# Optimization experiments

Measured on AMD Instinct MI355X. Metric: run time of the kernel, lower is better.

The kernel has to match this reference:

```python
import jax, jax.numpy as jnp
import numpy as np

N_NODES = 100000
N_EDGES = 3200000
D = 128
B = 4


def gcn_conv(x, row, col, W, b, n):
    # PyG GCNConv: x' = D^{-1/2}(A+I)D^{-1/2} (x W) + b
    xw = x @ W  # [N, out]
    ones = jnp.ones((row.shape[0],), dtype=x.dtype)
    deg = jax.ops.segment_sum(ones, col, num_segments=n) + 1.0  # self-loop
    dinv = jax.lax.rsqrt(deg)  # deg > 0 because of self-loops
    norm = dinv[row] * dinv[col]  # [E]
    msg = xw[row] * norm[:, None]  # gather + scale
    agg = jax.ops.segment_sum(msg, col, num_segments=n)  # scatter-add
    agg = agg + (dinv * dinv)[:, None] * xw  # self-loop contribution
    return agg + b


def setup_inputs() -> dict:
    key = jax.random.key(0)
    ks = jax.random.split(key, 10)
    x = jax.random.normal(ks[0], (N_NODES, D), dtype=jnp.float32)
    edge_index = jax.random.randint(ks[1], (2, N_EDGES), 0, N_NODES, dtype=jnp.int64)
    question_embeddings = jax.random.normal(ks[2], (B, D), dtype=jnp.float32)
    s = 1.0 / np.sqrt(D)
    W1 = jax.random.uniform(ks[3], (D, D), jnp.float32, -s, s)
    b1 = jnp.zeros((D,), jnp.float32)
    W2 = jax.random.uniform(ks[4], (D, D), jnp.float32, -s, s)
    b2 = jnp.zeros((D,), jnp.float32)
    Wq = jax.random.uniform(ks[5], (D, D), jnp.float32, -s, s)
    bq = jax.random.uniform(ks[6], (D,), jnp.float32, -s, s)
    return {"x": x, "edge_index": edge_index, "question_embeddings": question_embeddings,
            "W1": W1, "b1": b1, "W2": W2, "b2": b2, "Wq": Wq, "bq": bq}


def reference(x, edge_index, question_embeddings, W1, b1, W2, b2, Wq, bq):
    n = x.shape[0]
    row, col = edge_index[0], edge_index[1]
    h = jax.nn.relu(gcn_conv(x, row, col, W1, b1, n))  # [N, H]
    h = gcn_conv(h, row, col, W2, b2, n)  # [N, H]
    q = question_embeddings @ Wq + bq  # [B, H]
    out = h[None, :, :] + q[:, None, :]  # [B, N, H]
    return jax.nn.log_softmax(out, axis=1)  # softmax over node dim (torch dim=1)
```

## Files before the change

kernel.cpp:

```cpp
#include <hip/hip_runtime.h>
#include <math.h>

#define DD 128
#define CT 16384
#define CAP 10240

typedef unsigned int uint;
typedef unsigned short u16;

typedef __attribute__((ext_vector_type(8))) __bf16 bf16x8;
typedef __attribute__((ext_vector_type(2))) __bf16 bf16x2;
typedef __attribute__((ext_vector_type(4))) float f32x4;
typedef __attribute__((ext_vector_type(4))) uint uint4v;
typedef __attribute__((ext_vector_type(8))) u16 u16x8;


__device__ inline uint bf16bits(float a) {
  uint u = __float_as_uint(a);
  return (u + 0x7fffu + ((u >> 16) & 1u)) >> 16;
}

__device__ inline uint pack_bf16x2(float a, float b) {
  bf16x2 t;
  t[0] = (__bf16)a;
  t[1] = (__bf16)b;
  return __builtin_bit_cast(uint, t);
}

__device__ inline float lo16f(uint u) { return __uint_as_float(u << 16); }
__device__ inline float hi16f(uint u) { return __uint_as_float(u & 0xffff0000u); }


__global__ __launch_bounds__(256) void k_coarse(const int* __restrict__ row,
                                                const int* __restrict__ col,
                                                int* __restrict__ gcursor,
                                                uint* __restrict__ coarse,
                                                int E, int NB) {
  __shared__ int hist[512];
  __shared__ int base[512];
  int tid = threadIdx.x;
  long e0 = (long)blockIdx.x * CT;
  int cnt = (int)min((long)CT, (long)E - e0);
  int cnt4 = cnt >> 2;
  const int4* c4p = (const int4*)(col + e0);
  const int4* r4p = (const int4*)(row + e0);
  for (int i = tid; i < NB; i += 256) hist[i] = 0;
  __syncthreads();
  for (int i = tid; i < cnt4; i += 256) {
    int4 c = c4p[i];
    atomicAdd(&hist[c.x >> 8], 1);
    atomicAdd(&hist[c.y >> 8], 1);
    atomicAdd(&hist[c.z >> 8], 1);
    atomicAdd(&hist[c.w >> 8], 1);
  }
  for (int i = (cnt4 << 2) + tid; i < cnt; i += 256) atomicAdd(&hist[col[e0 + i] >> 8], 1);
  __syncthreads();
  for (int i = tid; i < NB; i += 256) {
    base[i] = i * CAP + atomicAdd(&gcursor[i], hist[i]);
    hist[i] = 0;
  }
  __syncthreads();
  for (int i = tid; i < cnt4; i += 256) {
    int4 c = c4p[i];
    int4 r = r4p[i];
    int b;
    b = c.x >> 8; coarse[base[b] + atomicAdd(&hist[b], 1)] = ((uint)r.x << 8) | (uint)(c.x & 255);
    b = c.y >> 8; coarse[base[b] + atomicAdd(&hist[b], 1)] = ((uint)r.y << 8) | (uint)(c.y & 255);
    b = c.z >> 8; coarse[base[b] + atomicAdd(&hist[b], 1)] = ((uint)r.z << 8) | (uint)(c.z & 255);
    b = c.w >> 8; coarse[base[b] + atomicAdd(&hist[b], 1)] = ((uint)r.w << 8) | (uint)(c.w & 255);
  }
  for (int i = (cnt4 << 2) + tid; i < cnt; i += 256) {
    int c = col[e0 + i];
    int r = row[e0 + i];
    int b = c >> 8;
    coarse[base[b] + atomicAdd(&hist[b], 1)] = ((uint)r << 8) | (uint)(c & 255);
  }
}

__global__ __launch_bounds__(256) void k_finalize(const uint* __restrict__ coarse,
                                                  const int* __restrict__ gcursor,
                                                  int* __restrict__ offB,
                                                  int* __restrict__ offE,
                                                  float* __restrict__ dinv,
                                                  int* __restrict__ srt, int n) {
  __shared__ int hist[256];
  __shared__ int s[256];
  __shared__ int cur[256];
  int tid = threadIdx.x;
  int b = blockIdx.x;
  int base = b * CAP;
  int cnt = gcursor[b];
  int cnt4 = cnt >> 2;
  const uint4* e4p = (const uint4*)(coarse + base);
  int node0 = b << 8;
  hist[tid] = 0;
  __syncthreads();
  for (int i = tid; i < cnt4; i += 256) {
    uint4 e = e4p[i];
    atomicAdd(&hist[e.x & 255u], 1);
    atomicAdd(&hist[e.y & 255u], 1);
    atomicAdd(&hist[e.z & 255u], 1);
    atomicAdd(&hist[e.w & 255u], 1);
  }
  for (int i = (cnt4 << 2) + tid; i < cnt; i += 256) atomicAdd(&hist[coarse[base + i] & 255u], 1);
  __syncthreads();
  int deg = hist[tid];
  s[tid] = deg;
  __syncthreads();
  for (int o = 1; o < 256; o <<= 1) {
    int add = (tid >= o) ? s[tid - o] : 0;
    __syncthreads();
    s[tid] += add;
    __syncthreads();
  }
  int p0 = base + s[tid] - deg;
  int node = node0 + tid;
  if (node < n) {
    offB[node] = p0;
    offE[node] = p0 + deg;
    dinv[node] = rsqrtf(1.0f + (float)deg);
  }
  cur[tid] = p0;
  __syncthreads();
  for (int i = tid; i < cnt4; i += 256) {
    uint4 e = e4p[i];
    int pos;
    pos = atomicAdd(&cur[e.x & 255u], 1); srt[pos] = (int)(e.x & 0xFFFFFF00u);
    pos = atomicAdd(&cur[e.y & 255u], 1); srt[pos] = (int)(e.y & 0xFFFFFF00u);
    pos = atomicAdd(&cur[e.z & 255u], 1); srt[pos] = (int)(e.z & 0xFFFFFF00u);
    pos = atomicAdd(&cur[e.w & 255u], 1); srt[pos] = (int)(e.w & 0xFFFFFF00u);
  }
  for (int i = (cnt4 << 2) + tid; i < cnt; i += 256) {
    uint e = coarse[base + i];
    int pos = atomicAdd(&cur[e & 255u], 1);
    srt[pos] = (int)(e & 0xFFFFFF00u);
  }
}


__global__ __launch_bounds__(256) void k_prepw(const float* __restrict__ W1,
                                               const float* __restrict__ W2,
                                               u16* __restrict__ o1h, u16* __restrict__ o1l,
                                               u16* __restrict__ o2h, u16* __restrict__ o2l,
                                               int* __restrict__ gcursor, int NB) {
  if (blockIdx.x == 0)
    for (int i = threadIdx.x; i < NB; i += 256) gcursor[i] = 0;
  const float* W = blockIdx.x ? W2 : W1;
  u16* oh = blockIdx.x ? o2h : o1h;
  u16* ol = blockIdx.x ? o2l : o1l;
  for (int i = threadIdx.x; i < 16384; i += 256) {
    int k = i >> 7, c = i & 127;
    float v = W[i];
    uint hb = bf16bits(v);
    float hv = __uint_as_float(hb << 16);
    uint lb = bf16bits(v - hv);
    uint uidx = (((uint)c << 6) + ((uint)k >> 1)) ^ (((uint)c & 7u) << 2);
    int p = (int)((uidx << 1) | ((uint)k & 1u));
    oh[p] = (u16)hb;
    ol[p] = (u16)lb;
  }
}


template <int PRE>
__global__ __launch_bounds__(256, 2) void k_gemm(const float* __restrict__ X,
                                                 const uint* __restrict__ Xh,
                                                 const uint* __restrict__ Xl,
                                                 const u16* __restrict__ gWh,
                                                 const u16* __restrict__ gWl,
                                                 const float* __restrict__ dinv,
                                                 uint* __restrict__ msg, int n) {
  __shared__ uint Wh[8192];
  __shared__ uint Wl[8192];
  int tid = threadIdx.x;
  for (int i = tid; i < 2048; i += 256) ((uint4*)Wh)[i] = ((const uint4*)gWh)[i];
  for (int i = tid; i < 2048; i += 256) ((uint4*)Wl)[i] = ((const uint4*)gWl)[i];

  int lane = tid & 63, wv = tid >> 6;
  int s_ = lane & 15, g = lane >> 4;
  int row0 = blockIdx.x * 128 + wv * 32;

  f32x4 acc[2][8];
#pragma unroll
  for (int a = 0; a < 2; a++)
#pragma unroll
    for (int b = 0; b < 8; b++) acc[a][b] = (f32x4)0.f;

  __syncthreads();

#pragma unroll
  for (int kc = 0; kc < 4; kc++) {
    uint4v ah[2], al[2];
#pragma unroll
    for (int sub = 0; sub < 2; sub++) {
      int r = row0 + sub * 16 + s_;
      if (PRE) {
        uint4 hv = make_uint4(0u, 0u, 0u, 0u), lv = hv;
        if (r < n) {
          hv = ((const uint4*)Xh)[(size_t)r * 16 + kc * 4 + g];
          lv = ((const uint4*)Xl)[(size_t)r * 16 + kc * 4 + g];
        }
        ah[sub][0] = hv.x; ah[sub][1] = hv.y; ah[sub][2] = hv.z; ah[sub][3] = hv.w;
        al[sub][0] = lv.x; al[sub][1] = lv.y; al[sub][2] = lv.z; al[sub][3] = lv.w;
      } else {
        float4 v0, v1;
        if (r < n) {
          const float* xp = X + (size_t)r * DD + kc * 32 + g * 8;
          v0 = ((const float4*)xp)[0];
          v1 = ((const float4*)xp)[1];
        } else {
          v0 = make_float4(0.f, 0.f, 0.f, 0.f);
          v1 = v0;
        }
        uint p0 = pack_bf16x2(v0.x, v0.y), p1 = pack_bf16x2(v0.z, v0.w);
        uint p2 = pack_bf16x2(v1.x, v1.y), p3 = pack_bf16x2(v1.z, v1.w);
        ah[sub][0] = p0; ah[sub][1] = p1; ah[sub][2] = p2; ah[sub][3] = p3;
        al[sub][0] = pack_bf16x2(v0.x - lo16f(p0), v0.y - hi16f(p0));
        al[sub][1] = pack_bf16x2(v0.z - lo16f(p1), v0.w - hi16f(p1));
        al[sub][2] = pack_bf16x2(v1.x - lo16f(p2), v1.y - hi16f(p2));
        al[sub][3] = pack_bf16x2(v1.z - lo16f(p3), v1.w - hi16f(p3));
      }
    }
    int koff2 = (kc * 32 + g * 8) >> 1;
#pragma unroll
    for (int ct = 0; ct < 8; ct++) {
      int c = ct * 16 + s_;
      int uo = (int)(((uint)(c << 6) + (uint)koff2) ^ (((uint)c & 7u) << 2));
      bf16x8 bh = __builtin_bit_cast(bf16x8, *(const u16x8*)&Wh[uo]);
      bf16x8 bl = __builtin_bit_cast(bf16x8, *(const u16x8*)&Wl[uo]);
#pragma unroll
      for (int sub = 0; sub < 2; sub++) {
        bf16x8 av = __builtin_bit_cast(bf16x8, ah[sub]);
        bf16x8 lv = __builtin_bit_cast(bf16x8, al[sub]);
        acc[sub][ct] = __builtin_amdgcn_mfma_f32_16x16x32_bf16(av, bh, acc[sub][ct], 0, 0, 0);
        acc[sub][ct] = __builtin_amdgcn_mfma_f32_16x16x32_bf16(lv, bh, acc[sub][ct], 0, 0, 0);
        acc[sub][ct] = __builtin_amdgcn_mfma_f32_16x16x32_bf16(av, bl, acc[sub][ct], 0, 0, 0);
      }
    }
  }

#pragma unroll
  for (int sub = 0; sub < 2; sub++) {
#pragma unroll
    for (int q = 0; q < 4; q++) {
      int rq = row0 + sub * 16 + g * 4 + q;
      if (rq < n) {
        float di = dinv[rq];
        uint* mrow = msg + (size_t)rq * 64;
#pragma unroll
        for (int ct = 0; ct < 4; ct++) {
          uint u = pack_bf16x2(acc[sub][ct][q] * di, acc[sub][ct + 4][q] * di);
          mrow[ct * 16 + s_] = u;
        }
      }
    }
  }
}


__global__ __launch_bounds__(256) void k_agg(const uint* __restrict__ msg,
                                             const int* __restrict__ srt,
                                             const int* __restrict__ offB,
                                             const int* __restrict__ offE,
                                             const float* __restrict__ dinv,
                                             const float* __restrict__ bias,
                                             float* __restrict__ out,
                                             uint* __restrict__ hh,
                                             uint* __restrict__ hl, int n, int relu) {
  int lane = threadIdx.x & 63;
  int s_ = lane & 15, g = lane >> 4;
  int node = blockIdx.x * 4 + (threadIdx.x >> 6);
  if (node >= n) return;
  int beg = offB[node], end = offE[node];
  float a0 = 0.f, a1 = 0.f, a2 = 0.f, a3 = 0.f, a4 = 0.f, a5 = 0.f, a6 = 0.f, a7 = 0.f;
  const char* mb = (const char*)msg + s_ * 16;
  for (int t = beg; t < end; t += 64) {
    int nt = end - t;
    if (nt > 64) nt = 64;
    int boff = srt[t + (lane < nt ? lane : nt - 1)];
    for (int k = 0; k < nt; k += 32) {
      uint4 r[8];
      if (k + 32 <= nt) {
#pragma unroll
        for (int u = 0; u < 8; u++) {
          int bo = __shfl(boff, k + u * 4 + g);
          r[u] = *(const uint4*)(mb + (uint)bo);
        }
#pragma unroll
        for (int u = 0; u < 8; u++) {
          a0 += __uint_as_float(r[u].x << 16); a4 += __uint_as_float(r[u].x & 0xffff0000u);
          a1 += __uint_as_float(r[u].y << 16); a5 += __uint_as_float(r[u].y & 0xffff0000u);
          a2 += __uint_as_float(r[u].z << 16); a6 += __uint_as_float(r[u].z & 0xffff0000u);
          a3 += __uint_as_float(r[u].w << 16); a7 += __uint_as_float(r[u].w & 0xffff0000u);
        }
      } else {
#pragma unroll
        for (int u = 0; u < 8; u++) {
          int e = k + u * 4 + g;
          int bo = __shfl(boff, e < nt ? e : nt - 1);
          r[u] = *(const uint4*)(mb + (uint)bo);
          if (e >= nt) r[u] = make_uint4(0u, 0u, 0u, 0u);
        }
#pragma unroll
        for (int u = 0; u < 8; u++) {
          a0 += __uint_as_float(r[u].x << 16); a4 += __uint_as_float(r[u].x & 0xffff0000u);
          a1 += __uint_as_float(r[u].y << 16); a5 += __uint_as_float(r[u].y & 0xffff0000u);
          a2 += __uint_as_float(r[u].z << 16); a6 += __uint_as_float(r[u].z & 0xffff0000u);
          a3 += __uint_as_float(r[u].w << 16); a7 += __uint_as_float(r[u].w & 0xffff0000u);
        }
      }
    }
  }
#define RED(x) x += __shfl_xor(x, 16); x += __shfl_xor(x, 32);
  RED(a0) RED(a1) RED(a2) RED(a3) RED(a4) RED(a5) RED(a6) RED(a7)
#undef RED
  const uint4* m4 = (const uint4*)msg;
  uint4 rs = m4[(size_t)node * 16 + s_];
  a0 += __uint_as_float(rs.x << 16); a4 += __uint_as_float(rs.x & 0xffff0000u);
  a1 += __uint_as_float(rs.y << 16); a5 += __uint_as_float(rs.y & 0xffff0000u);
  a2 += __uint_as_float(rs.z << 16); a6 += __uint_as_float(rs.z & 0xffff0000u);
  a3 += __uint_as_float(rs.w << 16); a7 += __uint_as_float(rs.w & 0xffff0000u);
  float di = dinv[node];
  if (g < 2) {
    float4 bv = ((const float4*)(bias + (g ? 64 : 0)))[s_];
    float o0, o1, o2, o3;
    if (g == 0) {
      o0 = di * a0 + bv.x; o1 = di * a1 + bv.y; o2 = di * a2 + bv.z; o3 = di * a3 + bv.w;
    } else {
      o0 = di * a4 + bv.x; o1 = di * a5 + bv.y; o2 = di * a6 + bv.z; o3 = di * a7 + bv.w;
    }
    if (relu) {
      o0 = fmaxf(o0, 0.f); o1 = fmaxf(o1, 0.f); o2 = fmaxf(o2, 0.f); o3 = fmaxf(o3, 0.f);
      uint h0 = pack_bf16x2(o0, o1), h1 = pack_bf16x2(o2, o3);
      uint l0 = pack_bf16x2(o0 - lo16f(h0), o1 - hi16f(h0));
      uint l1 = pack_bf16x2(o2 - lo16f(h1), o3 - hi16f(h1));
      int mb2 = node * 64 + (g ? 32 : 0) + 2 * s_;
      *(uint2*)(hh + mb2) = make_uint2(h0, h1);
      *(uint2*)(hl + mb2) = make_uint2(l0, l1);
    } else {
      *(float4*)(out + (size_t)node * DD + (g ? 64 : 0) + 4 * s_) = make_float4(o0, o1, o2, o3);
    }
  }
}


__global__ __launch_bounds__(256) void k_colstat(const float* __restrict__ h, int n,
                                                 float* __restrict__ PM,
                                                 float* __restrict__ PS) {
  __shared__ float sm[128], ss[128];
  int d = threadIdx.x & 127, sub = threadIdx.x >> 7;
  float m = -3.4e38f, s = 0.f;
  for (int r = blockIdx.x * 2 + sub; r < n; r += gridDim.x * 2) {
    float v = h[(size_t)r * DD + d];
    float nm = fmaxf(m, v);
    s = s * __expf(m - nm) + __expf(v - nm);
    m = nm;
  }
  if (sub) { sm[d] = m; ss[d] = s; }
  __syncthreads();
  if (!sub) {
    float m2 = sm[d], s2 = ss[d];
    float nm = fmaxf(m, m2);
    float so = s * __expf(m - nm) + s2 * __expf(m2 - nm);
    PM[blockIdx.x * 128 + d] = nm;
    PS[blockIdx.x * 128 + d] = so;
  }
}

__global__ __launch_bounds__(64) void k_lsemerge(const float* __restrict__ PM,
                                                 const float* __restrict__ PS,
                                                 float* __restrict__ L, int nb) {
  int d = blockIdx.x;
  int lane = threadIdx.x;
  float m = -3.4e38f, s = 0.f;
  for (int p = lane; p < nb; p += 64) {
    float m2 = PM[p * 128 + d], s2 = PS[p * 128 + d];
    float nm = fmaxf(m, m2);
    s = s * __expf(m - nm) + s2 * __expf(m2 - nm);
    m = nm;
  }
#pragma unroll
  for (int o = 1; o < 64; o <<= 1) {
    float m2 = __shfl_xor(m, o), s2 = __shfl_xor(s, o);
    float nm = fmaxf(m, m2);
    s = s * __expf(m - nm) + s2 * __expf(m2 - nm);
    m = nm;
  }
  if (lane == 0) L[d] = m + logf(s);
}


__global__ __launch_bounds__(256) void k_final(const float* __restrict__ h,
                                               const float* __restrict__ L,
                                               float* __restrict__ out, int n, int B) {
  int idx = blockIdx.x * 256 + threadIdx.x;
  int nd4 = n * 32;
  if (idx >= nd4) return;
  int c4 = idx & 31;
  float4 hv = ((const float4*)h)[idx];
  float4 lv = ((const float4*)L)[c4];
  float4 r = make_float4(hv.x - lv.x, hv.y - lv.y, hv.z - lv.z, hv.w - lv.w);
  float4* o = (float4*)out;
  for (int b = 0; b < B; b++) o[(size_t)idx + (size_t)b * nd4] = r;
}


extern "C" void kernel_launch(void* const* d_in, const int* in_sizes, int n_in,
                              void* d_out, int out_size, void* d_ws, size_t ws_size,
                              hipStream_t stream) {
  const float* x  = (const float*)d_in[0];
  const int*   ei = (const int*)d_in[1];
  const float* W1 = (const float*)d_in[3];
  const float* b1 = (const float*)d_in[4];
  const float* W2 = (const float*)d_in[5];
  const float* b2 = (const float*)d_in[6];

  int n = in_sizes[0] / DD;
  int E = in_sizes[1] / 2;
  int B = out_size / (n * DD);
  const int* row = ei;
  const int* col = ei + E;

  float* out = (float*)d_out;
  size_t nd = (size_t)n * DD;
  int NB = (n + 255) / 256;
  size_t CAPN = (size_t)NB * CAP;
  uint* hh = (uint*)out;
  uint* hl = hh + (size_t)n * 64;
  float* bufB = out + nd;
  int* srt = (int*)(out + 2 * nd);
  uint* coarse = (uint*)(srt + CAPN);
  uint* msg = (uint*)coarse;
  char* sm = (char*)(out + 3 * nd);
  auto alloc = [&](size_t bytes) -> char* {
    char* p = sm;
    sm += (bytes + 63) & ~(size_t)63;
    return p;
  };
  float* dinv = (float*)alloc(sizeof(float) * n);
  int* offB = (int*)alloc(sizeof(int) * n);
  int* offE = (int*)alloc(sizeof(int) * n);
  int* gcursor = (int*)alloc(sizeof(int) * NB);
  u16* wt1h = (u16*)alloc(32768);
  u16* wt1l = (u16*)alloc(32768);
  u16* wt2h = (u16*)alloc(32768);
  u16* wt2l = (u16*)alloc(32768);
  float* PM = (float*)alloc(sizeof(float) * 512 * 128);
  float* PS = (float*)alloc(sizeof(float) * 512 * 128);
  float* L = (float*)d_ws;

  int gC = (E + CT - 1) / CT;

  k_prepw<<<2, 256, 0, stream>>>(W1, W2, wt1h, wt1l, wt2h, wt2l, gcursor, NB);
  k_coarse<<<gC, 256, 0, stream>>>(row, col, gcursor, coarse, E, NB);
  k_finalize<<<NB, 256, 0, stream>>>(coarse, gcursor, offB, offE, dinv, srt, n);

  int gG = (n + 127) / 128;
  k_gemm<0><<<gG, 256, 0, stream>>>(x, nullptr, nullptr, wt1h, wt1l, dinv, msg, n);
  k_agg<<<(n + 3) / 4, 256, 0, stream>>>(msg, srt, offB, offE, dinv, b1, bufB, hh, hl, n, 1);
  k_gemm<1><<<gG, 256, 0, stream>>>(nullptr, hh, hl, wt2h, wt2l, dinv, msg, n);
  k_agg<<<(n + 3) / 4, 256, 0, stream>>>(msg, srt, offB, offE, dinv, b2, bufB, hh, hl, n, 0);

  k_colstat<<<512, 256, 0, stream>>>(bufB, n, PM, PS);
  k_lsemerge<<<128, 64, 0, stream>>>(PM, PS, L, 512);
  k_final<<<(n * 32 + 255) / 256, 256, 0, stream>>>(bufB, L, out, n, B);
}
```

Before: 676.9 us.

## Pre-sort bucket edges by source row in shared memory before CSR scatter

```diff
diff --git a/kernel.cpp b/kernel.cpp
--- a/kernel.cpp
+++ b/kernel.cpp
@@ -83,6 +83,7 @@
                                                   int* __restrict__ offE,
                                                   float* __restrict__ dinv,
                                                   int* __restrict__ srt, int n) {
+  __shared__ uint srtd[CAP];
   __shared__ int hist[256];
   __shared__ int s[256];
   __shared__ int cur[256];
@@ -93,16 +94,45 @@
   int cnt4 = cnt >> 2;
   const uint4* e4p = (const uint4*)(coarse + base);
   int node0 = b << 8;
+
   hist[tid] = 0;
   __syncthreads();
   for (int i = tid; i < cnt4; i += 256) {
     uint4 e = e4p[i];
-    atomicAdd(&hist[e.x & 255u], 1);
-    atomicAdd(&hist[e.y & 255u], 1);
-    atomicAdd(&hist[e.z & 255u], 1);
-    atomicAdd(&hist[e.w & 255u], 1);
-  }
-  for (int i = (cnt4 << 2) + tid; i < cnt; i += 256) atomicAdd(&hist[coarse[base + i] & 255u], 1);
+    atomicAdd(&hist[e.x >> 17], 1);
+    atomicAdd(&hist[e.y >> 17], 1);
+    atomicAdd(&hist[e.z >> 17], 1);
+    atomicAdd(&hist[e.w >> 17], 1);
+  }
+  for (int i = (cnt4 << 2) + tid; i < cnt; i += 256) atomicAdd(&hist[coarse[base + i] >> 17], 1);
+  __syncthreads();
+  int hA = hist[tid];
+  s[tid] = hA;
+  __syncthreads();
+  for (int o = 1; o < 256; o <<= 1) {
+    int add = (tid >= o) ? s[tid - o] : 0;
+    __syncthreads();
+    s[tid] += add;
+    __syncthreads();
+  }
+  cur[tid] = s[tid] - hA;
+  __syncthreads();
+  for (int i = tid; i < cnt4; i += 256) {
+    uint4 e = e4p[i];
+    srtd[atomicAdd(&cur[e.x >> 17], 1)] = e.x;
+    srtd[atomicAdd(&cur[e.y >> 17], 1)] = e.y;
+    srtd[atomicAdd(&cur[e.z >> 17], 1)] = e.z;
+    srtd[atomicAdd(&cur[e.w >> 17], 1)] = e.w;
+  }
+  for (int i = (cnt4 << 2) + tid; i < cnt; i += 256) {
+    uint e = coarse[base + i];
+    srtd[atomicAdd(&cur[e >> 17], 1)] = e;
+  }
+  __syncthreads();
+
+  hist[tid] = 0;
+  __syncthreads();
+  for (int i = tid; i < cnt; i += 256) atomicAdd(&hist[srtd[i] & 255u], 1);
   __syncthreads();
   int deg = hist[tid];
   s[tid] = deg;
@@ -122,16 +152,8 @@
   }
   cur[tid] = p0;
   __syncthreads();
-  for (int i = tid; i < cnt4; i += 256) {
-    uint4 e = e4p[i];
-    int pos;
-    pos = atomicAdd(&cur[e.x & 255u], 1); srt[pos] = (int)(e.x & 0xFFFFFF00u);
-    pos = atomicAdd(&cur[e.y & 255u], 1); srt[pos] = (int)(e.y & 0xFFFFFF00u);
-    pos = atomicAdd(&cur[e.z & 255u], 1); srt[pos] = (int)(e.z & 0xFFFFFF00u);
-    pos = atomicAdd(&cur[e.w & 255u], 1); srt[pos] = (int)(e.w & 0xFFFFFF00u);
-  }
-  for (int i = (cnt4 << 2) + tid; i < cnt; i += 256) {
-    uint e = coarse[base + i];
+  for (int i = tid; i < cnt; i += 256) {
+    uint e = srtd[i];
     int pos = atomicAdd(&cur[e & 255u], 1);
     srt[pos] = (int)(e & 0xFFFFFF00u);
   }
```

Measured after the change: 680.5 us. No clear change (+0.5%).
